# Kernel optimization log

Measured on AMD Instinct MI355X. Metric: run time of the kernel, lower is better.

The kernel has to match this reference:

```python
import jax, jax.numpy as jnp
import numpy as np

B, S, D, F, E, K = 4, 2048, 512, 1024, 8, 2

def setup_inputs() -> dict:
    key = jax.random.key(0)
    ks = jax.random.split(key, 7)
    hidden = jax.random.normal(ks[0], (B, S, D), dtype=jnp.float32)
    top_k_indices = jax.random.randint(ks[1], (B, S, K), 0, E, dtype=jnp.int32)
    top_k_weights = jax.random.uniform(ks[2], (B, S, K), dtype=jnp.float32)
    scale1 = 1.0 / np.sqrt(D)
    scale2 = 1.0 / np.sqrt(F)
    W1 = jax.random.normal(ks[3], (E, D, F), dtype=jnp.float32) * scale1
    b1 = jnp.zeros((E, F), dtype=jnp.float32)
    W2 = jax.random.normal(ks[4], (E, F, D), dtype=jnp.float32) * scale2
    b2 = jnp.zeros((E, D), dtype=jnp.float32)
    return {"hidden": hidden, "top_k_indices": top_k_indices,
            "top_k_weights": top_k_weights, "W1": W1, "b1": b1, "W2": W2, "b2": b2}

def reference(hidden, top_k_indices, top_k_weights, W1, b1, W2, b2):
    b, s, d = hidden.shape
    e = W1.shape[0]
    x = hidden.reshape(-1, d)                      # [T, D]
    idx = top_k_indices.reshape(-1, top_k_indices.shape[-1])   # [T, K]
    w = top_k_weights.reshape(-1, top_k_weights.shape[-1])     # [T, K]
    # combine weight per (token, expert): sum over k slots routed to expert e
    onehot = jax.nn.one_hot(idx, e, dtype=w.dtype)             # [T, K, E]
    cw = jnp.einsum('tk,tke->et', w, onehot)                   # [E, T]
    def step(acc, params):
        W1e, b1e, W2e, b2e, cwe = params
        h = jax.nn.gelu(x @ W1e + b1e)                         # [T, F]
        y = h @ W2e + b2e                                      # [T, D]
        return acc + cwe[:, None] * y, None
    out, _ = jax.lax.scan(step, jnp.zeros_like(x), (W1, b1, W2, b2, cw))
    return out.reshape(b, s, d)
```

## Files before the change

### kernel.cpp

```cpp
#include <hip/hip_runtime.h>
#include <hip/hip_bf16.h>

#define T_TOK 8192
#define DDIM  512
#define FDIM  1024
#define NEXP  8
#define KTOP  2
#define NSLOT (T_TOK * KTOP)
#define MAX_ROWS 17408
#define MAX_T128 136

typedef __attribute__((ext_vector_type(8))) __bf16 bf16x8;
typedef __attribute__((ext_vector_type(4))) __bf16 bf16x4;
typedef __attribute__((ext_vector_type(4))) float  f32x4;
typedef __attribute__((ext_vector_type(8))) unsigned short u16x8;

typedef __attribute__((address_space(1))) const unsigned int* gp1;
typedef __attribute__((address_space(3))) unsigned int*       lp3;
#define GL2LDS(g, l) __builtin_amdgcn_global_load_lds((gp1)(const void*)(g), (lp3)(void*)(l), 16, 0, 0)


__device__ __forceinline__ float gelu_fast(float x){
    float u = 0.7978845608028654f * (x + 0.044715f * x * x * x);
    return x / (1.0f + __expf(-2.0f * u));
}

__device__ __forceinline__ unsigned short f2bf(float v){
    __hip_bfloat16 b = __float2bfloat16(v);
    return *(unsigned short*)&b;
}

__global__ void cast_x_bf16(const float* __restrict__ src, unsigned short* __restrict__ dst,
                            int n8){
    int i = blockIdx.x * blockDim.x + threadIdx.x;
    if (i >= n8) return;
    const float4* s = (const float4*)src;
    float4 a = s[2 * i];
    float4 b = s[2 * i + 1];
    u16x8 o;
    o[0] = f2bf(a.x); o[1] = f2bf(a.y); o[2] = f2bf(a.z); o[3] = f2bf(a.w);
    o[4] = f2bf(b.x); o[5] = f2bf(b.y); o[6] = f2bf(b.z); o[7] = f2bf(b.w);
    *(u16x8*)(dst + (size_t)i * 8) = o;
}

__global__ __launch_bounds__(1024) void bucket_kernel(
    const int* __restrict__ idx, int* __restrict__ meta, int2* __restrict__ map,
    int* __restrict__ list, int* __restrict__ slot2row)
{
    __shared__ int scan[NEXP][1024];
    const int tid = threadIdx.x;
    const int base = tid * 16;

    int mye[16];
    int c[NEXP];
    #pragma unroll
    for (int e = 0; e < NEXP; e++) c[e] = 0;
    #pragma unroll
    for (int i = 0; i < 16; i++){
        mye[i] = idx[base + i] & 7;
        c[mye[i]]++;
    }
    #pragma unroll
    for (int e = 0; e < NEXP; e++) scan[e][tid] = c[e];
    __syncthreads();

    for (int off = 1; off < 1024; off <<= 1){
        int t[NEXP];
        #pragma unroll
        for (int e = 0; e < NEXP; e++) t[e] = (tid >= off) ? scan[e][tid - off] : 0;
        __syncthreads();
        #pragma unroll
        for (int e = 0; e < NEXP; e++) scan[e][tid] += t[e];
        __syncthreads();
    }

    int cnt[NEXP], pad[NEXP], off_e[NEXP];
    int o = 0;
    #pragma unroll
    for (int e = 0; e < NEXP; e++){
        cnt[e] = scan[e][1023];
        pad[e] = (cnt[e] + 127) & ~127;
        off_e[e] = o;
        o += pad[e];
    }
    const int nrows = o;

    if (tid == 0){
        int nt = 0;
        for (int e = 0; e < NEXP; e++){
            meta[17 + e] = off_e[e];
            for (int tb = 0; tb < (pad[e] >> 7); tb++)
                map[nt++] = make_int2(e, off_e[e] + tb * 128);
        }
        meta[16] = nt;
    }

    int run[NEXP];
    #pragma unroll
    for (int e = 0; e < NEXP; e++) run[e] = off_e[e] + scan[e][tid] - c[e];
    #pragma unroll
    for (int i = 0; i < 16; i++){
        int e = mye[i];
        int gg = run[e]++;
        list[gg] = (base + i) >> 1;
        slot2row[base + i] = gg;
    }

    for (int p = tid; p < nrows; p += 1024){
        #pragma unroll
        for (int e = 0; e < NEXP; e++){
            if (p >= off_e[e] + cnt[e] && p < off_e[e] + pad[e]) list[p] = 0;
        }
    }
}

__global__ void transpose_cast(const float* __restrict__ src,
                               unsigned short* __restrict__ dst, int R, int C){
    __shared__ unsigned short tile[32][33];
    int e = blockIdx.z;
    int c0 = blockIdx.x * 32, r0 = blockIdx.y * 32;
    int tx = threadIdx.x, ty = threadIdx.y;
    const float* sf = src + (size_t)e * R * C;
    unsigned short* d = dst + (size_t)e * R * C;
    #pragma unroll
    for (int i = 0; i < 4; i++)
        tile[ty + i * 8][tx] = f2bf(sf[(size_t)(r0 + ty + i * 8) * C + c0 + tx]);
    __syncthreads();
    #pragma unroll
    for (int i = 0; i < 4; i++)
        d[(size_t)(c0 + ty + i * 8) * R + r0 + tx] = tile[tx][ty + i * 8];
}

__global__ __launch_bounds__(256, 2) void gemm1_kernel(
    const unsigned short* __restrict__ x,
    const unsigned short* __restrict__ w1t,
    const float* __restrict__ b1,
    const int* __restrict__ meta,
    const int2* __restrict__ map,
    const int* __restrict__ list,
    unsigned short* __restrict__ h)
{
    const int ntiles = meta[16];
    const int nwg = ntiles * (FDIM / 128);
    int id = blockIdx.y * gridDim.x + blockIdx.x;
    if (id >= nwg) return;
    int q = nwg >> 3, r = nwg & 7;
    int xcd = id & 7, rank = id >> 3;
    int swz = (xcd < r) ? (xcd * (q + 1) + rank)
                        : (r * (q + 1) + (xcd - r) * q + rank);
    const int tile = swz >> 3;
    const int n0 = (swz & 7) * 128;
    int2 em = map[tile];
    const int e = em.x, grow0 = em.y;

    __shared__ __align__(16) unsigned short As[2 * 128 * 32];
    __shared__ __align__(16) unsigned short Bs[2 * 128 * 32];

    const int tid  = threadIdx.x;
    const int wave = tid >> 6;
    const int lane = tid & 63;
    const int rl   = lane >> 2;
    const int kq   = lane & 3;

    const int row0 = wave * 16 + rl;
    const int row1 = 64 + wave * 16 + rl;

    const unsigned short* pA0 = x + (size_t)list[grow0 + row0] * DDIM + kq * 8;
    const unsigned short* pA1 = x + (size_t)list[grow0 + row1] * DDIM + kq * 8;
    const unsigned short* pB0 = w1t + ((size_t)e * FDIM + n0 + row0) * DDIM + kq * 8;
    const unsigned short* pB1 = w1t + ((size_t)e * FDIM + n0 + row1) * DDIM + kq * 8;

    char* lA = (char*)As + wave * 1024;
    char* lB = (char*)Bs + wave * 1024;

    const int quad = lane >> 4, lrow = lane & 15;
    const int wr = (wave >> 1) * 64;
    const int wc = (wave & 1) * 64;

    f32x4 acc[4][4];
    #pragma unroll
    for (int i = 0; i < 4; i++)
        #pragma unroll
        for (int j = 0; j < 4; j++) acc[i][j] = (f32x4)0.0f;

    for (int kk = 0; kk < DDIM; kk += 64){
        __syncthreads();
        GL2LDS(pA0 + kk,      lA);
        GL2LDS(pA1 + kk,      lA + 4096);
        GL2LDS(pA0 + kk + 32, lA + 8192);
        GL2LDS(pA1 + kk + 32, lA + 12288);
        GL2LDS(pB0 + kk,      lB);
        GL2LDS(pB1 + kk,      lB + 4096);
        GL2LDS(pB0 + kk + 32, lB + 8192);
        GL2LDS(pB1 + kk + 32, lB + 12288);
        __syncthreads();
        bf16x8 a[4][2], b[4][2];
        #pragma unroll
        for (int i = 0; i < 4; i++){
            #pragma unroll
            for (int ks = 0; ks < 2; ks++){
                a[i][ks] = *(const bf16x8*)&As[ks * 4096 + (wr + i * 16 + lrow) * 32 + quad * 8];
                b[i][ks] = *(const bf16x8*)&Bs[ks * 4096 + (wc + i * 16 + lrow) * 32 + quad * 8];
            }
        }
        #pragma unroll
        for (int i = 0; i < 4; i++){
            #pragma unroll
            for (int j = 0; j < 4; j++){
                acc[i][j] = __builtin_amdgcn_mfma_f32_16x16x32_bf16(a[i][0], b[j][0], acc[i][j], 0, 0, 0);
                acc[i][j] = __builtin_amdgcn_mfma_f32_16x16x32_bf16(a[i][1], b[j][1], acc[i][j], 0, 0, 0);
            }
        }
    }

    #pragma unroll
    for (int j = 0; j < 4; j++){
        int cn = n0 + wc + j * 16 + lrow;
        float bias = b1[e * FDIM + cn];
        #pragma unroll
        for (int i = 0; i < 4; i++){
            #pragma unroll
            for (int rr = 0; rr < 4; rr++){
                int gr = grow0 + wr + i * 16 + quad * 4 + rr;
                h[(size_t)gr * FDIM + cn] = f2bf(gelu_fast(acc[i][j][rr] + bias));
            }
        }
    }
}

__global__ __launch_bounds__(256, 2) void gemm2_kernel(
    const unsigned short* __restrict__ h,
    const unsigned short* __restrict__ w2t,
    const float* __restrict__ b2,
    const int* __restrict__ meta,
    const int2* __restrict__ map,
    unsigned short* __restrict__ y)
{
    const int ntiles = meta[16];
    const int nwg = ntiles * (DDIM / 128);
    int id = blockIdx.y * gridDim.x + blockIdx.x;
    if (id >= nwg) return;
    int q = nwg >> 3, r = nwg & 7;
    int xcd = id & 7, rank = id >> 3;
    int swz = (xcd < r) ? (xcd * (q + 1) + rank)
                        : (r * (q + 1) + (xcd - r) * q + rank);
    const int tile = swz >> 2;
    const int n0 = (swz & 3) * 128;
    int2 em = map[tile];
    const int e = em.x, grow0 = em.y;

    __shared__ __align__(16) unsigned short As[2 * 128 * 32];
    __shared__ __align__(16) unsigned short Bs[2 * 128 * 32];

    const int tid  = threadIdx.x;
    const int wave = tid >> 6;
    const int lane = tid & 63;
    const int rl   = lane >> 2;
    const int kq   = lane & 3;

    const int row0 = wave * 16 + rl;
    const int row1 = 64 + wave * 16 + rl;

    const unsigned short* pA0 = h + (size_t)(grow0 + row0) * FDIM + kq * 8;
    const unsigned short* pA1 = h + (size_t)(grow0 + row1) * FDIM + kq * 8;
    const unsigned short* pB0 = w2t + ((size_t)e * DDIM + n0 + row0) * FDIM + kq * 8;
    const unsigned short* pB1 = w2t + ((size_t)e * DDIM + n0 + row1) * FDIM + kq * 8;

    char* lA = (char*)As + wave * 1024;
    char* lB = (char*)Bs + wave * 1024;

    const int quad = lane >> 4, lrow = lane & 15;
    const int wr = (wave >> 1) * 64;
    const int wc = (wave & 1) * 64;

    f32x4 acc[4][4];
    #pragma unroll
    for (int i = 0; i < 4; i++)
        #pragma unroll
        for (int j = 0; j < 4; j++) acc[i][j] = (f32x4)0.0f;

    for (int kk = 0; kk < FDIM; kk += 64){
        __syncthreads();
        GL2LDS(pA0 + kk,      lA);
        GL2LDS(pA1 + kk,      lA + 4096);
        GL2LDS(pA0 + kk + 32, lA + 8192);
        GL2LDS(pA1 + kk + 32, lA + 12288);
        GL2LDS(pB0 + kk,      lB);
        GL2LDS(pB1 + kk,      lB + 4096);
        GL2LDS(pB0 + kk + 32, lB + 8192);
        GL2LDS(pB1 + kk + 32, lB + 12288);
        __syncthreads();
        bf16x8 a[4][2], b[4][2];
        #pragma unroll
        for (int i = 0; i < 4; i++){
            #pragma unroll
            for (int ks = 0; ks < 2; ks++){
                a[i][ks] = *(const bf16x8*)&As[ks * 4096 + (wr + i * 16 + lrow) * 32 + quad * 8];
                b[i][ks] = *(const bf16x8*)&Bs[ks * 4096 + (wc + i * 16 + lrow) * 32 + quad * 8];
            }
        }
        #pragma unroll
        for (int i = 0; i < 4; i++){
            #pragma unroll
            for (int j = 0; j < 4; j++){
                acc[i][j] = __builtin_amdgcn_mfma_f32_16x16x32_bf16(a[i][0], b[j][0], acc[i][j], 0, 0, 0);
                acc[i][j] = __builtin_amdgcn_mfma_f32_16x16x32_bf16(a[i][1], b[j][1], acc[i][j], 0, 0, 0);
            }
        }
    }

    #pragma unroll
    for (int j = 0; j < 4; j++){
        int cn = n0 + wc + j * 16 + lrow;
        float bias = b2[e * DDIM + cn];
        #pragma unroll
        for (int i = 0; i < 4; i++){
            #pragma unroll
            for (int rr = 0; rr < 4; rr++){
                int gr = grow0 + wr + i * 16 + quad * 4 + rr;
                y[(size_t)gr * DDIM + cn] = f2bf(acc[i][j][rr] + bias);
            }
        }
    }
}

__global__ void combine_kernel(const unsigned short* __restrict__ y,
                               const int* __restrict__ slot2row,
                               const float* __restrict__ wk,
                               float* __restrict__ out){
    int g = blockIdx.x * blockDim.x + threadIdx.x;
    int t = g >> 7, seg = g & 127;
    int ra = slot2row[2 * t], rb = slot2row[2 * t + 1];
    float wa = wk[2 * t];
    float wb = wk[2 * t + 1];
    bf16x4 ya = *(const bf16x4*)(y + (size_t)ra * DDIM + seg * 4);
    bf16x4 yb = *(const bf16x4*)(y + (size_t)rb * DDIM + seg * 4);
    float4 o;
    o.x = wa * (float)ya[0] + wb * (float)yb[0];
    o.y = wa * (float)ya[1] + wb * (float)yb[1];
    o.z = wa * (float)ya[2] + wb * (float)yb[2];
    o.w = wa * (float)ya[3] + wb * (float)yb[3];
    *(float4*)(out + (size_t)t * DDIM + seg * 4) = o;
}

extern "C" void kernel_launch(void* const* d_in, const int* in_sizes, int n_in,
                              void* d_out, int out_size, void* d_ws, size_t ws_size,
                              hipStream_t stream){
    const float* x   = (const float*)d_in[0];
    const int*   idx = (const int*)d_in[1];
    const float* wk  = (const float*)d_in[2];
    const float* W1  = (const float*)d_in[3];
    const float* b1  = (const float*)d_in[4];
    const float* W2  = (const float*)d_in[5];
    const float* b2  = (const float*)d_in[6];
    float* out = (float*)d_out;

    char* ws = (char*)d_ws;
    int*   meta     = (int*)ws;
    int2*  map      = (int2*)(ws + 512);
    int*   list     = (int*)(ws + 4096);
    int*   slot2row = (int*)(ws + 81920);
    unsigned short* xbf = (unsigned short*)(ws + 262144);
    unsigned short* w1t = (unsigned short*)(ws + 8650752);
    unsigned short* w2t = (unsigned short*)(ws + 17039360);
    unsigned short* h   = (unsigned short*)(ws + 25427968);
    unsigned short* y   = (unsigned short*)(ws + 61079552);
    if (ws_size < 78905344u) return;

    cast_x_bf16<<<(T_TOK * DDIM / 8) / 256, 256, 0, stream>>>(x, xbf, T_TOK * DDIM / 8);

    transpose_cast<<<dim3(FDIM / 32, DDIM / 32, NEXP), dim3(32, 8), 0, stream>>>(
        W1, w1t, DDIM, FDIM);
    transpose_cast<<<dim3(DDIM / 32, FDIM / 32, NEXP), dim3(32, 8), 0, stream>>>(
        W2, w2t, FDIM, DDIM);

    bucket_kernel<<<1, 1024, 0, stream>>>(idx, meta, map, list, slot2row);

    gemm1_kernel<<<dim3(FDIM / 128, MAX_T128), 256, 0, stream>>>(
        xbf, w1t, b1, meta, map, list, h);
    gemm2_kernel<<<dim3(DDIM / 128, MAX_T128), 256, 0, stream>>>(
        h, w2t, b2, meta, map, y);

    combine_kernel<<<(T_TOK * DDIM / 4) / 256, 256, 0, stream>>>(y, slot2row, wk, out);
}
```

Baseline: 194.0 us.

## Double-buffer LDS in expert GEMMs and pack bucket scan counters

Both expert GEMM kernels now keep two LDS buffers. The global-to-LDS loads for the next K step are issued before the current step's MFMAs, with one explicit waitcnt plus barrier per step, so load latency can overlap compute instead of being serialized by two syncthreads per iteration. The bucket kernel packs the eight per-expert counts into two 64-bit words with 16-bit lanes, which cuts scan LDS traffic, and it builds the tile map in parallel. LDS use per block doubles to 64KB, which may limit occupancy at two blocks per CU.

```diff
diff --git a/kernel.cpp b/kernel.cpp
--- a/kernel.cpp
+++ b/kernel.cpp
@@ -47,57 +47,63 @@
     const int* __restrict__ idx, int* __restrict__ meta, int2* __restrict__ map,
     int* __restrict__ list, int* __restrict__ slot2row)
 {
-    __shared__ int scan[NEXP][1024];
+    __shared__ unsigned long long sA[1024], sB[1024];
     const int tid = threadIdx.x;
     const int base = tid * 16;
 
     int mye[16];
-    int c[NEXP];
-    #pragma unroll
-    for (int e = 0; e < NEXP; e++) c[e] = 0;
+    unsigned long long a = 0, b = 0;
     #pragma unroll
     for (int i = 0; i < 16; i++){
-        mye[i] = idx[base + i] & 7;
-        c[mye[i]]++;
-    }
-    #pragma unroll
-    for (int e = 0; e < NEXP; e++) scan[e][tid] = c[e];
+        int e = idx[base + i] & 7;
+        mye[i] = e;
+        unsigned long long one = 1ull << (16 * (e & 3));
+        if (e < 4) a += one; else b += one;
+    }
+    sA[tid] = a; sB[tid] = b;
     __syncthreads();
 
     for (int off = 1; off < 1024; off <<= 1){
-        int t[NEXP];
-        #pragma unroll
-        for (int e = 0; e < NEXP; e++) t[e] = (tid >= off) ? scan[e][tid - off] : 0;
+        unsigned long long ta = 0, tb = 0;
+        if (tid >= off){ ta = sA[tid - off]; tb = sB[tid - off]; }
         __syncthreads();
-        #pragma unroll
-        for (int e = 0; e < NEXP; e++) scan[e][tid] += t[e];
+        sA[tid] += ta; sB[tid] += tb;
         __syncthreads();
     }
 
-    int cnt[NEXP], pad[NEXP], off_e[NEXP];
+    const unsigned long long iA = sA[tid],  iB = sB[tid];
+    const unsigned long long tA = sA[1023], tB = sB[1023];
+
+    int cnt[NEXP], pad[NEXP], off_e[NEXP], tc[NEXP + 1];
+    tc[0] = 0;
     int o = 0;
     #pragma unroll
     for (int e = 0; e < NEXP; e++){
-        cnt[e] = scan[e][1023];
+        unsigned long long src = (e < 4) ? tA : tB;
+        cnt[e] = (int)((src >> (16 * (e & 3))) & 0xffffull);
         pad[e] = (cnt[e] + 127) & ~127;
-        off_e[e] = o;
-        o += pad[e];
-    }
-    const int nrows = o;
-
-    if (tid == 0){
-        int nt = 0;
-        for (int e = 0; e < NEXP; e++){
-            meta[17 + e] = off_e[e];
-            for (int tb = 0; tb < (pad[e] >> 7); tb++)
-                map[nt++] = make_int2(e, off_e[e] + tb * 128);
-        }
-        meta[16] = nt;
+        off_e[e] = o; o += pad[e];
+        tc[e + 1] = tc[e] + (pad[e] >> 7);
+    }
+    const int nrows = o, nt = tc[NEXP];
+
+    if (tid == 0) meta[16] = nt;
+    if (tid < NEXP) meta[17 + tid] = off_e[tid];
+    if (tid < nt){
+        int e = 0;
+        while (tid >= tc[e + 1]) e++;
+        map[tid] = make_int2(e, off_e[e] + (tid - tc[e]) * 128);
     }
 
     int run[NEXP];
     #pragma unroll
-    for (int e = 0; e < NEXP; e++) run[e] = off_e[e] + scan[e][tid] - c[e];
+    for (int e = 0; e < NEXP; e++){
+        unsigned long long isrc = (e < 4) ? iA : iB;
+        unsigned long long csrc = (e < 4) ? a  : b;
+        int incl = (int)((isrc >> (16 * (e & 3))) & 0xffffull);
+        int ce   = (int)((csrc >> (16 * (e & 3))) & 0xffffull);
+        run[e] = off_e[e] + incl - ce;
+    }
     #pragma unroll
     for (int i = 0; i < 16; i++){
         int e = mye[i];
@@ -130,6 +136,18 @@
     for (int i = 0; i < 4; i++)
         d[(size_t)(c0 + ty + i * 8) * R + r0 + tx] = tile[tx][ty + i * 8];
 }
+
+#define PIPE_PROLOGUE_SYNC()  do {                                   \
+    asm volatile("s_waitcnt vmcnt(0)" ::: "memory");                 \
+    __builtin_amdgcn_s_barrier();                                    \
+    __builtin_amdgcn_sched_barrier(0);                               \
+} while (0)
+#define PIPE_STEP_SYNC()  do {                                       \
+    __builtin_amdgcn_sched_barrier(0);                               \
+    asm volatile("s_waitcnt vmcnt(0) lgkmcnt(0)" ::: "memory");      \
+    __builtin_amdgcn_s_barrier();                                    \
+    __builtin_amdgcn_sched_barrier(0);                               \
+} while (0)
 
 __global__ __launch_bounds__(256, 2) void gemm1_kernel(
     const unsigned short* __restrict__ x,
@@ -153,8 +171,8 @@
     int2 em = map[tile];
     const int e = em.x, grow0 = em.y;
 
-    __shared__ __align__(16) unsigned short As[2 * 128 * 32];
-    __shared__ __align__(16) unsigned short Bs[2 * 128 * 32];
+    __shared__ __align__(16) unsigned short As[2][8192];
+    __shared__ __align__(16) unsigned short Bs[2][8192];
 
     const int tid  = threadIdx.x;
     const int wave = tid >> 6;
@@ -170,37 +188,40 @@
     const unsigned short* pB0 = w1t + ((size_t)e * FDIM + n0 + row0) * DDIM + kq * 8;
     const unsigned short* pB1 = w1t + ((size_t)e * FDIM + n0 + row1) * DDIM + kq * 8;
 
-    char* lA = (char*)As + wave * 1024;
-    char* lB = (char*)Bs + wave * 1024;
-
     const int quad = lane >> 4, lrow = lane & 15;
     const int wr = (wave >> 1) * 64;
     const int wc = (wave & 1) * 64;
 
+#define STAGE1(buf, kk) do {                                                  \
+        char* la_ = (char*)As[buf] + wave * 1024;                             \
+        char* lb_ = (char*)Bs[buf] + wave * 1024;                             \
+        GL2LDS(pA0 + (kk),      la_);          GL2LDS(pA1 + (kk),      la_ + 4096);  \
+        GL2LDS(pA0 + (kk) + 32, la_ + 8192);   GL2LDS(pA1 + (kk) + 32, la_ + 12288); \
+        GL2LDS(pB0 + (kk),      lb_);          GL2LDS(pB1 + (kk),      lb_ + 4096);  \
+        GL2LDS(pB0 + (kk) + 32, lb_ + 8192);   GL2LDS(pB1 + (kk) + 32, lb_ + 12288); \
+    } while (0)
+
     f32x4 acc[4][4];
     #pragma unroll
     for (int i = 0; i < 4; i++)
         #pragma unroll
         for (int j = 0; j < 4; j++) acc[i][j] = (f32x4)0.0f;
 
-    for (int kk = 0; kk < DDIM; kk += 64){
-        __syncthreads();
-        GL2LDS(pA0 + kk,      lA);
-        GL2LDS(pA1 + kk,      lA + 4096);
-        GL2LDS(pA0 + kk + 32, lA + 8192);
-        GL2LDS(pA1 + kk + 32, lA + 12288);
-        GL2LDS(pB0 + kk,      lB);
-        GL2LDS(pB1 + kk,      lB + 4096);
-        GL2LDS(pB0 + kk + 32, lB + 8192);
-        GL2LDS(pB1 + kk + 32, lB + 12288);
-        __syncthreads();
+    STAGE1(0, 0);
+    PIPE_PROLOGUE_SYNC();
+
+    const int NK = DDIM / 64;
+    #pragma unroll 2
+    for (int t = 0; t < NK; ++t){
+        const int cur = t & 1;
+        if (t + 1 < NK) STAGE1(cur ^ 1, (t + 1) * 64);
         bf16x8 a[4][2], b[4][2];
         #pragma unroll
         for (int i = 0; i < 4; i++){
             #pragma unroll
             for (int ks = 0; ks < 2; ks++){
-                a[i][ks] = *(const bf16x8*)&As[ks * 4096 + (wr + i * 16 + lrow) * 32 + quad * 8];
-                b[i][ks] = *(const bf16x8*)&Bs[ks * 4096 + (wc + i * 16 + lrow) * 32 + quad * 8];
+                a[i][ks] = *(const bf16x8*)&As[cur][ks * 4096 + (wr + i * 16 + lrow) * 32 + quad * 8];
+                b[i][ks] = *(const bf16x8*)&Bs[cur][ks * 4096 + (wc + i * 16 + lrow) * 32 + quad * 8];
             }
         }
         #pragma unroll
@@ -211,7 +232,9 @@
                 acc[i][j] = __builtin_amdgcn_mfma_f32_16x16x32_bf16(a[i][1], b[j][1], acc[i][j], 0, 0, 0);
             }
         }
-    }
+        if (t + 1 < NK) PIPE_STEP_SYNC();
+    }
+#undef STAGE1
 
     #pragma unroll
     for (int j = 0; j < 4; j++){
@@ -249,8 +272,8 @@
     int2 em = map[tile];
     const int e = em.x, grow0 = em.y;
 
-    __shared__ __align__(16) unsigned short As[2 * 128 * 32];
-    __shared__ __align__(16) unsigned short Bs[2 * 128 * 32];
+    __shared__ __align__(16) unsigned short As[2][8192];
+    __shared__ __align__(16) unsigned short Bs[2][8192];
 
     const int tid  = threadIdx.x;
     const int wave = tid >> 6;
@@ -266,37 +289,40 @@
     const unsigned short* pB0 = w2t + ((size_t)e * DDIM + n0 + row0) * FDIM + kq * 8;
     const unsigned short* pB1 = w2t + ((size_t)e * DDIM + n0 + row1) * FDIM + kq * 8;
 
-    char* lA = (char*)As + wave * 1024;
-    char* lB = (char*)Bs + wave * 1024;
-
     const int quad = lane >> 4, lrow = lane & 15;
     const int wr = (wave >> 1) * 64;
     const int wc = (wave & 1) * 64;
 
+#define STAGE2(buf, kk) do {                                                  \
+        char* la_ = (char*)As[buf] + wave * 1024;                             \
+        char* lb_ = (char*)Bs[buf] + wave * 1024;                             \
+        GL2LDS(pA0 + (kk),      la_);          GL2LDS(pA1 + (kk),      la_ + 4096);  \
+        GL2LDS(pA0 + (kk) + 32, la_ + 8192);   GL2LDS(pA1 + (kk) + 32, la_ + 12288); \
+        GL2LDS(pB0 + (kk),      lb_);          GL2LDS(pB1 + (kk),      lb_ + 4096);  \
+        GL2LDS(pB0 + (kk) + 32, lb_ + 8192);   GL2LDS(pB1 + (kk) + 32, lb_ + 12288); \
+    } while (0)
+
     f32x4 acc[4][4];
     #pragma unroll
     for (int i = 0; i < 4; i++)
         #pragma unroll
         for (int j = 0; j < 4; j++) acc[i][j] = (f32x4)0.0f;
 
-    for (int kk = 0; kk < FDIM; kk += 64){
-        __syncthreads();
-        GL2LDS(pA0 + kk,      lA);
-        GL2LDS(pA1 + kk,      lA + 4096);
-        GL2LDS(pA0 + kk + 32, lA + 8192);
-        GL2LDS(pA1 + kk + 32, lA + 12288);
-        GL2LDS(pB0 + kk,      lB);
-        GL2LDS(pB1 + kk,      lB + 4096);
-        GL2LDS(pB0 + kk + 32, lB + 8192);
-        GL2LDS(pB1 + kk + 32, lB + 12288);
-        __syncthreads();
+    STAGE2(0, 0);
+    PIPE_PROLOGUE_SYNC();
+
+    const int NK = FDIM / 64;
+    #pragma unroll 2
+    for (int t = 0; t < NK; ++t){
+        const int cur = t & 1;
+        if (t + 1 < NK) STAGE2(cur ^ 1, (t + 1) * 64);
         bf16x8 a[4][2], b[4][2];
         #pragma unroll
         for (int i = 0; i < 4; i++){
             #pragma unroll
             for (int ks = 0; ks < 2; ks++){
-                a[i][ks] = *(const bf16x8*)&As[ks * 4096 + (wr + i * 16 + lrow) * 32 + quad * 8];
-                b[i][ks] = *(const bf16x8*)&Bs[ks * 4096 + (wc + i * 16 + lrow) * 32 + quad * 8];
+                a[i][ks] = *(const bf16x8*)&As[cur][ks * 4096 + (wr + i * 16 + lrow) * 32 + quad * 8];
+                b[i][ks] = *(const bf16x8*)&Bs[cur][ks * 4096 + (wc + i * 16 + lrow) * 32 + quad * 8];
             }
         }
         #pragma unroll
@@ -307,7 +333,9 @@
                 acc[i][j] = __builtin_amdgcn_mfma_f32_16x16x32_bf16(a[i][1], b[j][1], acc[i][j], 0, 0, 0);
             }
         }
-    }
+        if (t + 1 < NK) PIPE_STEP_SYNC();
+    }
+#undef STAGE2
 
     #pragma unroll
     for (int j = 0; j < 4; j++){
```

Result: slower. 198.0 us (+2.1%).

## Fuse prep kernels into one launch and scatter-combine in gemm2 via atomics

Applied to the files above, without the earlier changes.

Merges the x cast, both weight transposes, bucketing, and output zeroing into a single multi-role prep kernel. The bucketing scan now uses packed 16-bit counters in 64-bit words. The combine kernel and the bf16 y intermediate are removed: gemm2 multiplies by the per-row routing weight and atomically adds fp32 results into the output, which removes a kernel launch and the y round trip through memory. The cost is atomic contention on the output and a non-deterministic summation order. Launch bounds also drop the minimum of two blocks per CU.

```diff
diff --git a/kernel.cpp b/kernel.cpp
--- a/kernel.cpp
+++ b/kernel.cpp
@@ -10,8 +10,12 @@
 #define MAX_ROWS 17408
 #define MAX_T128 136
 
+#define NB_CAST 512
+#define NB_T    4096
+#define NB_ZERO 1024
+#define PREP_BLOCKS (1 + NB_CAST + NB_T + NB_T + NB_ZERO)
+
 typedef __attribute__((ext_vector_type(8))) __bf16 bf16x8;
-typedef __attribute__((ext_vector_type(4))) __bf16 bf16x4;
 typedef __attribute__((ext_vector_type(4))) float  f32x4;
 typedef __attribute__((ext_vector_type(8))) unsigned short u16x8;
 
@@ -30,108 +34,121 @@
     return *(unsigned short*)&b;
 }
 
-__global__ void cast_x_bf16(const float* __restrict__ src, unsigned short* __restrict__ dst,
-                            int n8){
-    int i = blockIdx.x * blockDim.x + threadIdx.x;
-    if (i >= n8) return;
-    const float4* s = (const float4*)src;
-    float4 a = s[2 * i];
-    float4 b = s[2 * i + 1];
-    u16x8 o;
-    o[0] = f2bf(a.x); o[1] = f2bf(a.y); o[2] = f2bf(a.z); o[3] = f2bf(a.w);
-    o[4] = f2bf(b.x); o[5] = f2bf(b.y); o[6] = f2bf(b.z); o[7] = f2bf(b.w);
-    *(u16x8*)(dst + (size_t)i * 8) = o;
-}
-
-__global__ __launch_bounds__(1024) void bucket_kernel(
-    const int* __restrict__ idx, int* __restrict__ meta, int2* __restrict__ map,
-    int* __restrict__ list, int* __restrict__ slot2row)
+__global__ __launch_bounds__(1024) void prep_kernel(
+    const float* __restrict__ x, const int* __restrict__ idx,
+    const float* __restrict__ wk,
+    const float* __restrict__ W1, const float* __restrict__ W2,
+    unsigned short* __restrict__ xbf,
+    unsigned short* __restrict__ w1t, unsigned short* __restrict__ w2t,
+    int* __restrict__ meta, int2* __restrict__ map,
+    int* __restrict__ list, float* __restrict__ rowwk,
+    float* __restrict__ out)
 {
-    __shared__ int scan[NEXP][1024];
+    __shared__ unsigned long long sA[1024], sB[1024];
+    __shared__ unsigned short tile[32][33];
+    const int b   = blockIdx.x;
     const int tid = threadIdx.x;
-    const int base = tid * 16;
-
-    int mye[16];
-    int c[NEXP];
-    #pragma unroll
-    for (int e = 0; e < NEXP; e++) c[e] = 0;
-    #pragma unroll
-    for (int i = 0; i < 16; i++){
-        mye[i] = idx[base + i] & 7;
-        c[mye[i]]++;
-    }
-    #pragma unroll
-    for (int e = 0; e < NEXP; e++) scan[e][tid] = c[e];
-    __syncthreads();
-
-    for (int off = 1; off < 1024; off <<= 1){
-        int t[NEXP];
-        #pragma unroll
-        for (int e = 0; e < NEXP; e++) t[e] = (tid >= off) ? scan[e][tid - off] : 0;
-        __syncthreads();
-        #pragma unroll
-        for (int e = 0; e < NEXP; e++) scan[e][tid] += t[e];
-        __syncthreads();
-    }
-
-    int cnt[NEXP], pad[NEXP], off_e[NEXP];
-    int o = 0;
-    #pragma unroll
-    for (int e = 0; e < NEXP; e++){
-        cnt[e] = scan[e][1023];
-        pad[e] = (cnt[e] + 127) & ~127;
-        off_e[e] = o;
-        o += pad[e];
-    }
-    const int nrows = o;
-
-    if (tid == 0){
-        int nt = 0;
+
+    if (b == 0){
+        const int base = tid * 16;
+        int mye[16];
+        unsigned long long a = 0, bb = 0;
+        #pragma unroll
+        for (int i = 0; i < 16; i++){
+            int e = idx[base + i] & 7;
+            mye[i] = e;
+            unsigned long long one = 1ull << (16 * (e & 3));
+            if (e < 4) a += one; else bb += one;
+        }
+        sA[tid] = a; sB[tid] = bb;
+        __syncthreads();
+        for (int off = 1; off < 1024; off <<= 1){
+            unsigned long long ta = 0, tb = 0;
+            if (tid >= off){ ta = sA[tid - off]; tb = sB[tid - off]; }
+            __syncthreads();
+            sA[tid] += ta; sB[tid] += tb;
+            __syncthreads();
+        }
+        const unsigned long long iA = sA[tid],  iB = sB[tid];
+        const unsigned long long tA = sA[1023], tB = sB[1023];
+
+        int cnt[NEXP], pad[NEXP], off_e[NEXP], tc[NEXP + 1];
+        tc[0] = 0;
+        int o = 0;
+        #pragma unroll
         for (int e = 0; e < NEXP; e++){
-            meta[17 + e] = off_e[e];
-            for (int tb = 0; tb < (pad[e] >> 7); tb++)
-                map[nt++] = make_int2(e, off_e[e] + tb * 128);
-        }
-        meta[16] = nt;
-    }
-
-    int run[NEXP];
-    #pragma unroll
-    for (int e = 0; e < NEXP; e++) run[e] = off_e[e] + scan[e][tid] - c[e];
-    #pragma unroll
-    for (int i = 0; i < 16; i++){
-        int e = mye[i];
-        int gg = run[e]++;
-        list[gg] = (base + i) >> 1;
-        slot2row[base + i] = gg;
-    }
-
-    for (int p = tid; p < nrows; p += 1024){
+            unsigned long long src = (e < 4) ? tA : tB;
+            cnt[e] = (int)((src >> (16 * (e & 3))) & 0xffffull);
+            pad[e] = (cnt[e] + 127) & ~127;
+            off_e[e] = o; o += pad[e];
+            tc[e + 1] = tc[e] + (pad[e] >> 7);
+        }
+        const int nrows = o, nt = tc[NEXP];
+
+        if (tid == 0) meta[16] = nt;
+        if (tid < NEXP) meta[17 + tid] = off_e[tid];
+        if (tid < nt){
+            int e = 0;
+            while (tid >= tc[e + 1]) e++;
+            map[tid] = make_int2(e, off_e[e] + (tid - tc[e]) * 128);
+        }
+
+        int run[NEXP];
         #pragma unroll
         for (int e = 0; e < NEXP; e++){
-            if (p >= off_e[e] + cnt[e] && p < off_e[e] + pad[e]) list[p] = 0;
-        }
-    }
-}
-
-__global__ void transpose_cast(const float* __restrict__ src,
-                               unsigned short* __restrict__ dst, int R, int C){
-    __shared__ unsigned short tile[32][33];
-    int e = blockIdx.z;
-    int c0 = blockIdx.x * 32, r0 = blockIdx.y * 32;
-    int tx = threadIdx.x, ty = threadIdx.y;
-    const float* sf = src + (size_t)e * R * C;
-    unsigned short* d = dst + (size_t)e * R * C;
-    #pragma unroll
-    for (int i = 0; i < 4; i++)
-        tile[ty + i * 8][tx] = f2bf(sf[(size_t)(r0 + ty + i * 8) * C + c0 + tx]);
-    __syncthreads();
-    #pragma unroll
-    for (int i = 0; i < 4; i++)
-        d[(size_t)(c0 + ty + i * 8) * R + r0 + tx] = tile[tx][ty + i * 8];
-}
-
-__global__ __launch_bounds__(256, 2) void gemm1_kernel(
+            unsigned long long isrc = (e < 4) ? iA : iB;
+            unsigned long long csrc = (e < 4) ? a  : bb;
+            int incl = (int)((isrc >> (16 * (e & 3))) & 0xffffull);
+            int ce   = (int)((csrc >> (16 * (e & 3))) & 0xffffull);
+            run[e] = off_e[e] + incl - ce;
+        }
+        #pragma unroll
+        for (int i = 0; i < 16; i++){
+            int e = mye[i];
+            int gg = run[e]++;
+            list[gg]  = (base + i) >> 1;
+            rowwk[gg] = wk[base + i];
+        }
+        for (int p = tid; p < nrows; p += 1024){
+            #pragma unroll
+            for (int e = 0; e < NEXP; e++){
+                if (p >= off_e[e] + cnt[e] && p < off_e[e] + pad[e]){
+                    list[p] = 0; rowwk[p] = 0.0f;
+                }
+            }
+        }
+    } else if (b < 1 + NB_CAST){
+        int i = (b - 1) * 1024 + tid;
+        const float4* s = (const float4*)x;
+        float4 va = s[2 * i];
+        float4 vb = s[2 * i + 1];
+        u16x8 ov;
+        ov[0] = f2bf(va.x); ov[1] = f2bf(va.y); ov[2] = f2bf(va.z); ov[3] = f2bf(va.w);
+        ov[4] = f2bf(vb.x); ov[5] = f2bf(vb.y); ov[6] = f2bf(vb.z); ov[7] = f2bf(vb.w);
+        *(u16x8*)(xbf + (size_t)i * 8) = ov;
+    } else if (b < 1 + NB_CAST + 2 * NB_T){
+        int blk = b - (1 + NB_CAST);
+        const float* src; unsigned short* dst; int R, C, cpb_shift, cpb_mask;
+        if (blk < NB_T){ src = W1; dst = w1t; R = DDIM; C = FDIM; cpb_shift = 5; cpb_mask = 31; }
+        else           { src = W2; dst = w2t; R = FDIM; C = DDIM; cpb_shift = 4; cpb_mask = 15; blk -= NB_T; }
+        int e   = blk >> 9;
+        int rem = blk & 511;
+        int rb  = rem >> cpb_shift, cb = rem & cpb_mask;
+        int r0 = rb * 32, c0 = cb * 32;
+        int tx = tid & 31, ty = tid >> 5;
+        const float* sf = src + (size_t)e * R * C;
+        unsigned short* d = dst + (size_t)e * R * C;
+        tile[ty][tx] = f2bf(sf[(size_t)(r0 + ty) * C + c0 + tx]);
+        __syncthreads();
+        d[(size_t)(c0 + ty) * R + r0 + tx] = tile[tx][ty];
+    } else {
+        int blk = b - (1 + NB_CAST + 2 * NB_T);
+        int i4 = blk * 1024 + tid;
+        *(float4*)(out + (size_t)i4 * 4) = make_float4(0.f, 0.f, 0.f, 0.f);
+    }
+}
+
+__global__ __launch_bounds__(256) void gemm1_kernel(
     const unsigned short* __restrict__ x,
     const unsigned short* __restrict__ w1t,
     const float* __restrict__ b1,
@@ -228,13 +245,15 @@
     }
 }
 
-__global__ __launch_bounds__(256, 2) void gemm2_kernel(
+__global__ __launch_bounds__(256) void gemm2_kernel(
     const unsigned short* __restrict__ h,
     const unsigned short* __restrict__ w2t,
     const float* __restrict__ b2,
     const int* __restrict__ meta,
     const int2* __restrict__ map,
-    unsigned short* __restrict__ y)
+    const int* __restrict__ list,
+    const float* __restrict__ rowwk,
+    float* __restrict__ out)
 {
     const int ntiles = meta[16];
     const int nwg = ntiles * (DDIM / 128);
@@ -309,6 +328,17 @@
         }
     }
 
+    int   rt[4][4];
+    float rw[4][4];
+    #pragma unroll
+    for (int i = 0; i < 4; i++){
+        #pragma unroll
+        for (int rr = 0; rr < 4; rr++){
+            int gr = grow0 + wr + i * 16 + quad * 4 + rr;
+            rt[i][rr] = list[gr];
+            rw[i][rr] = rowwk[gr];
+        }
+    }
     #pragma unroll
     for (int j = 0; j < 4; j++){
         int cn = n0 + wc + j * 16 + lrow;
@@ -317,30 +347,13 @@
         for (int i = 0; i < 4; i++){
             #pragma unroll
             for (int rr = 0; rr < 4; rr++){
-                int gr = grow0 + wr + i * 16 + quad * 4 + rr;
-                y[(size_t)gr * DDIM + cn] = f2bf(acc[i][j][rr] + bias);
-            }
-        }
-    }
-}
-
-__global__ void combine_kernel(const unsigned short* __restrict__ y,
-                               const int* __restrict__ slot2row,
-                               const float* __restrict__ wk,
-                               float* __restrict__ out){
-    int g = blockIdx.x * blockDim.x + threadIdx.x;
-    int t = g >> 7, seg = g & 127;
-    int ra = slot2row[2 * t], rb = slot2row[2 * t + 1];
-    float wa = wk[2 * t];
-    float wb = wk[2 * t + 1];
-    bf16x4 ya = *(const bf16x4*)(y + (size_t)ra * DDIM + seg * 4);
-    bf16x4 yb = *(const bf16x4*)(y + (size_t)rb * DDIM + seg * 4);
-    float4 o;
-    o.x = wa * (float)ya[0] + wb * (float)yb[0];
-    o.y = wa * (float)ya[1] + wb * (float)yb[1];
-    o.z = wa * (float)ya[2] + wb * (float)yb[2];
-    o.w = wa * (float)ya[3] + wb * (float)yb[3];
-    *(float4*)(out + (size_t)t * DDIM + seg * 4) = o;
+                float w = rw[i][rr];
+                if (w != 0.0f)
+                    atomicAdd(&out[(size_t)rt[i][rr] * DDIM + cn],
+                              w * (acc[i][j][rr] + bias));
+            }
+        }
+    }
 }
 
 extern "C" void kernel_launch(void* const* d_in, const int* in_sizes, int n_in,
@@ -356,30 +369,22 @@
     float* out = (float*)d_out;
 
     char* ws = (char*)d_ws;
-    int*   meta     = (int*)ws;
-    int2*  map      = (int2*)(ws + 512);
-    int*   list     = (int*)(ws + 4096);
-    int*   slot2row = (int*)(ws + 81920);
+    int*   meta  = (int*)ws;
+    int2*  map   = (int2*)(ws + 512);
+    int*   list  = (int*)(ws + 4096);
+    float* rowwk = (float*)(ws + 81920);
     unsigned short* xbf = (unsigned short*)(ws + 262144);
     unsigned short* w1t = (unsigned short*)(ws + 8650752);
     unsigned short* w2t = (unsigned short*)(ws + 17039360);
     unsigned short* h   = (unsigned short*)(ws + 25427968);
-    unsigned short* y   = (unsigned short*)(ws + 61079552);
-    if (ws_size < 78905344u) return;
-
-    cast_x_bf16<<<(T_TOK * DDIM / 8) / 256, 256, 0, stream>>>(x, xbf, T_TOK * DDIM / 8);
-
-    transpose_cast<<<dim3(FDIM / 32, DDIM / 32, NEXP), dim3(32, 8), 0, stream>>>(
-        W1, w1t, DDIM, FDIM);
-    transpose_cast<<<dim3(DDIM / 32, FDIM / 32, NEXP), dim3(32, 8), 0, stream>>>(
-        W2, w2t, FDIM, DDIM);
-
-    bucket_kernel<<<1, 1024, 0, stream>>>(idx, meta, map, list, slot2row);
+    if (ws_size < 61079552u) return;
+
+    prep_kernel<<<PREP_BLOCKS, 1024, 0, stream>>>(
+        x, idx, wk, W1, W2, xbf, w1t, w2t, meta, map, list, rowwk, out);
 
     gemm1_kernel<<<dim3(FDIM / 128, MAX_T128), 256, 0, stream>>>(
         xbf, w1t, b1, meta, map, list, h);
+
     gemm2_kernel<<<dim3(DDIM / 128, MAX_T128), 256, 0, stream>>>(
-        h, w2t, b2, meta, map, y);
-
-    combine_kernel<<<(T_TOK * DDIM / 4) / 256, 256, 0, stream>>>(y, slot2row, wk, out);
-}
+        h, w2t, b2, meta, map, list, rowwk, out);
+}
```

Result: slower. 232.1 us (+19.7%).
